# Kernel optimization log

Measured on AMD Instinct MI355X. Metric: run time of the kernel, lower is better.

The kernel has to match this reference:

```python
import jax, jax.numpy as jnp
import numpy as np

N = 16384
K = 16

def _w(k, shape):
    return jax.random.normal(k, shape, jnp.float32) * 0.05

def setup_inputs() -> dict:
    key = jax.random.key(0)
    ks = jax.random.split(key, 20)
    return {
        "img_feat": jax.random.normal(ks[0], (1, 32, N), jnp.float32),
        "cloud": jax.random.uniform(ks[1], (1, N, 3), jnp.float32),
        "conv1_w": _w(ks[2], (64, 32)),   "conv1_b": _w(ks[3], (64,)),
        "conv2_w": _w(ks[4], (128, 64)),  "conv2_b": _w(ks[5], (128,)),
        "psconv1_w": _w(ks[6], (256, 128)), "psconv1_b": _w(ks[7], (256,)),
        "psconv2_w": _w(ks[8], (128, 256)), "psconv2_b": _w(ks[9], (128,)),
        "pconv1_w": _w(ks[10], (64, 3)),  "pconv1_b": _w(ks[11], (64,)),
        "pconv2_w": _w(ks[12], (128, 64)),"pconv2_b": _w(ks[13], (128,)),
        "final_w": _w(ks[14], (32, 416)), "final_b": _w(ks[15], (32,)),
        "topk": K,
    }

def reference(img_feat, cloud, conv1_w, conv1_b, conv2_w, conv2_b,
              psconv1_w, psconv1_b, psconv2_w, psconv2_b,
              pconv1_w, pconv1_b, pconv2_w, pconv2_b,
              final_w, final_b, topk):
    lrelu = lambda x: jax.nn.leaky_relu(x, 0.01)
    pts = cloud[0]            # [N,3]  (module assumes bs=1)
    imf = img_feat[0].T       # [N,32]
    # point MLP: pconv1 -> lrelu -> pconv2 (Conv1d kernel=1 == per-point linear)
    cf = lrelu(pts @ pconv1_w.T + pconv1_b) @ pconv2_w.T + pconv2_b  # [N,128]
    # KNN: k smallest euclidean distances (self included)
    sq = jnp.sum(pts * pts, axis=-1)                 # [N]
    d2 = sq[:, None] + sq[None, :] - 2.0 * (pts @ pts.T)  # [N,N]
    _, idx = jax.lax.top_k(-d2, topk)                # [N,K]
    nb_pts = pts[idx]                                # [N,K,3]
    dist = jnp.sqrt(jnp.maximum(jnp.sum((pts[:, None, :] - nb_pts) ** 2, -1), 1e-12))
    wgt = jax.nn.softmax(-dist, axis=1)              # [N,K]
    nb_img = imf[idx]                                # [N,K,32]
    nb_cf = cf[idx]                                  # [N,K,128]
    sf = lrelu(nb_img @ conv1_w.T + conv1_b) @ conv2_w.T + conv2_b         # [N,K,128]
    sfp = lrelu(nb_cf @ psconv1_w.T + psconv1_b) @ psconv2_w.T + psconv2_b # [N,K,128]
    sf = jnp.max(sf * wgt[:, :, None], axis=1)       # weighted max-pool -> [N,128]
    sfp = jnp.max(sfp * wgt[:, :, None], axis=1)     # [N,128]
    final = jnp.concatenate([sfp, imf, sf, cf], axis=1)  # [N,416]
    out = lrelu(final) @ final_w.T + final_b         # [N,32]
    return out.T[None]                               # [1,32,N]
```

## Files before the change

kernel.cpp:

```cpp
#include <hip/hip_runtime.h>
#include <math.h>

#define N 16384
#define KNN 16
#define G 14
#define NCELL (G * G * G)

typedef __attribute__((ext_vector_type(8))) short bf16x8;
typedef __attribute__((ext_vector_type(4))) float f32x4;
typedef unsigned short ushort_t;
typedef unsigned long long u64;

__device__ __forceinline__ float lrelu(float a) { return a > 0.f ? a : 0.01f * a; }

__device__ __forceinline__ ushort_t f2bf(float f) {
  unsigned u = __float_as_uint(f);
  u += 0x7FFF + ((u >> 16) & 1);
  return (ushort_t)(u >> 16);
}
__device__ __forceinline__ float bf2f(ushort_t h) {
  return __uint_as_float((unsigned)h << 16);
}
__device__ __forceinline__ float bflo(unsigned u) {
  return __uint_as_float(u << 16);
}
__device__ __forceinline__ float bfhi(unsigned u) {
  return __uint_as_float(u & 0xffff0000u);
}
__device__ __forceinline__ int lanerank(u64 mask) {
  return __builtin_amdgcn_mbcnt_hi((unsigned)(mask >> 32),
         __builtin_amdgcn_mbcnt_lo((unsigned)mask, 0));
}
__device__ __forceinline__ int cellof(float x) {
  int c = (int)(x * (float)G);
  return c < 0 ? 0 : (c > G - 1 ? G - 1 : c);
}
__device__ __forceinline__ int cellid(float x, float y, float z) {
  return (cellof(z) * G + cellof(y)) * G + cellof(x);
}

#define PPB 64
__global__ __launch_bounds__(256) void prepw_kernel(
    const float* __restrict__ img, const float* __restrict__ cloud,
    const float* __restrict__ p1w, const float* __restrict__ p1b,
    const float* __restrict__ p2w, const float* __restrict__ p2b,
    const float* __restrict__ ps1w, const float* __restrict__ ps2w,
    const float* __restrict__ c1w, const float* __restrict__ c2w,
    const float* __restrict__ fw,
    float4* __restrict__ pts4, ushort_t* __restrict__ cfh,
    ushort_t* __restrict__ imfh,
    ushort_t* __restrict__ w1h, ushort_t* __restrict__ w2h,
    ushort_t* __restrict__ c1h, ushort_t* __restrict__ c2h,
    ushort_t* __restrict__ fwh, int* __restrict__ count) {
  int t = threadIdx.x;
  if (blockIdx.x >= 256) {
    int e = (blockIdx.x - 256) * 256 + t;
    if (e < 32768) w1h[e] = f2bf(ps1w[e]);
    else if (e < 65536) w2h[e - 32768] = f2bf(ps2w[e - 32768]);
    else if (e < 67584) c1h[e - 65536] = f2bf(c1w[e - 65536]);
    else if (e < 75776) c2h[e - 67584] = f2bf(c2w[e - 67584]);
    else if (e < 89088) {
      int e2 = e - 75776;
      if (e2 < 13312) fwh[e2] = f2bf(fw[e2]);
    }
    return;
  }
  __shared__ alignas(16) float w2t[64 * 132];
  __shared__ alignas(16) float hs[PPB * 68];
  __shared__ alignas(16) float w1s[192];
  __shared__ alignas(16) float b1s[64];
  __shared__ alignas(16) float b2s[128];
  __shared__ alignas(16) ushort_t imt[PPB * 40];
  __shared__ float ptmp[PPB * 3];
  __shared__ float psx[PPB], psy[PPB], psz[PPB];
  int pb = blockIdx.x * PPB;

  for (int e = t; e < 128 * 64; e += 256) {
    int ch = e >> 6, k = e & 63;
    w2t[k * 132 + ch] = p2w[e];
  }
  if (t < 192) w1s[t] = p1w[t];
  if (t < 64) b1s[t] = p1b[t];
  if (t < 128) b2s[t] = p2b[t];
  if (t < PPB * 3) ptmp[t] = cloud[pb * 3 + t];
  __syncthreads();
  if (t < PPB) {
    float x = ptmp[t * 3], y = ptmp[t * 3 + 1], z = ptmp[t * 3 + 2];
    psx[t] = x; psy[t] = y; psz[t] = z;
    pts4[pb + t] = make_float4(x, y, z, x * x + y * y + z * z);
    atomicAdd(&count[cellid(x, y, z)], 1);
  }
  for (int e = t; e < 32 * PPB; e += 256) {
    int c = e >> 6, p = e & 63;
    imt[p * 40 + c] = f2bf(img[(size_t)c * N + pb + p]);
  }
  __syncthreads();
  {
    int p = t >> 2, c8 = (t & 3) << 3;
    *(uint4*)&imfh[(size_t)(pb + p) * 32 + c8] =
        *(const uint4*)&imt[p * 40 + c8];
  }
  for (int e = t; e < PPB * 64; e += 256) {
    int pt_ = e >> 6, ch = e & 63;
    float a = b1s[ch] + psx[pt_] * w1s[ch * 3] + psy[pt_] * w1s[ch * 3 + 1] +
              psz[pt_] * w1s[ch * 3 + 2];
    hs[pt_ * 68 + ch] = lrelu(a);
  }
  __syncthreads();
  for (int e = t; e < PPB * 32; e += 256) {
    int pt_ = e >> 5, c4 = (e & 31) << 2;
    float4 acc = *(const float4*)&b2s[c4];
    const float* hrow = &hs[pt_ * 68];
    #pragma unroll
    for (int k = 0; k < 64; k += 4) {
      float4 h4 = *(const float4*)&hrow[k];
      float4 w0 = *(const float4*)&w2t[(k + 0) * 132 + c4];
      float4 w1_ = *(const float4*)&w2t[(k + 1) * 132 + c4];
      float4 w2_ = *(const float4*)&w2t[(k + 2) * 132 + c4];
      float4 w3 = *(const float4*)&w2t[(k + 3) * 132 + c4];
      acc.x = fmaf(h4.x, w0.x, fmaf(h4.y, w1_.x, fmaf(h4.z, w2_.x, fmaf(h4.w, w3.x, acc.x))));
      acc.y = fmaf(h4.x, w0.y, fmaf(h4.y, w1_.y, fmaf(h4.z, w2_.y, fmaf(h4.w, w3.y, acc.y))));
      acc.z = fmaf(h4.x, w0.z, fmaf(h4.y, w1_.z, fmaf(h4.z, w2_.z, fmaf(h4.w, w3.z, acc.z))));
      acc.w = fmaf(h4.x, w0.w, fmaf(h4.y, w1_.w, fmaf(h4.z, w2_.w, fmaf(h4.w, w3.w, acc.w))));
    }
    unsigned lo = (unsigned)f2bf(acc.x) | ((unsigned)f2bf(acc.y) << 16);
    unsigned hi = (unsigned)f2bf(acc.z) | ((unsigned)f2bf(acc.w) << 16);
    *(uint2*)&cfh[(size_t)(pb + pt_) * 128 + c4] = make_uint2(lo, hi);
  }
}

__global__ __launch_bounds__(256) void scan_kernel(
    const int* __restrict__ count, int* __restrict__ cellStart,
    int* __restrict__ cellofs) {
  __shared__ int part[256];
  int t = threadIdx.x;
  int local[11];
  int s = 0;
  #pragma unroll
  for (int j = 0; j < 11; ++j) {
    int idx = t * 11 + j;
    local[j] = s;
    s += (idx < NCELL) ? count[idx] : 0;
  }
  part[t] = s;
  __syncthreads();
  for (int off = 1; off < 256; off <<= 1) {
    int v = (t >= off) ? part[t - off] : 0;
    __syncthreads();
    part[t] += v;
    __syncthreads();
  }
  int base = part[t] - s;
  #pragma unroll
  for (int j = 0; j < 11; ++j) {
    int idx = t * 11 + j;
    int v = base + local[j];
    if (idx < NCELL) { cellStart[idx] = v; cellofs[idx] = v; }
  }
  if (t == 255) cellStart[NCELL] = part[255];
}

__global__ __launch_bounds__(256) void scatter_kernel(
    const float4* __restrict__ pts4, int* __restrict__ cellofs,
    float4* __restrict__ spts) {
  int p = blockIdx.x * 256 + threadIdx.x;
  float4 v = pts4[p];
  int pos = atomicAdd(&cellofs[cellid(v.x, v.y, v.z)], 1);
  spts[pos] = make_float4(v.x, v.y, v.z, __int_as_float(p));
}

#define NB_LD 136
#define S1_LD 264
#define NI_LD 40
#define H1_LD 72
__global__ __launch_bounds__(256) void ymlp_kernel(
    const ushort_t* __restrict__ cfh, const ushort_t* __restrict__ imfh,
    const ushort_t* __restrict__ w1h, const float* __restrict__ b1,
    const ushort_t* __restrict__ w2h, const float* __restrict__ b2,
    const ushort_t* __restrict__ c1h, const float* __restrict__ c1b,
    const ushort_t* __restrict__ c2h, const float* __restrict__ c2b,
    ushort_t* __restrict__ ycf, ushort_t* __restrict__ yimg) {
  __shared__ alignas(16) ushort_t nb[64 * NB_LD];
  __shared__ alignas(16) ushort_t s1[64 * S1_LD];
  int t = threadIdx.x;
  int w = t >> 6, lane = t & 63;
  int col = lane & 15, quad = lane >> 4;

  if (blockIdx.x < 256) {
    int pbase = blockIdx.x * 64;
    for (int e = t; e < 1024; e += 256) {
      int row = e >> 4, c8 = (e & 15) << 3;
      *(uint4*)&nb[row * NB_LD + c8] =
          *(const uint4*)&cfh[(size_t)(pbase + row) * 128 + c8];
    }
    __syncthreads();
    f32x4 acc1[4][4];
    #pragma unroll
    for (int tt = 0; tt < 4; ++tt)
      #pragma unroll
      for (int p = 0; p < 4; ++p) acc1[tt][p] = (f32x4){0.f, 0.f, 0.f, 0.f};
    for (int k0 = 0; k0 < 128; k0 += 32) {
      bf16x8 a[4];
      #pragma unroll
      for (int p = 0; p < 4; ++p)
        a[p] = *(const bf16x8*)&nb[(p * 16 + col) * NB_LD + k0 + quad * 8];
      #pragma unroll
      for (int tt = 0; tt < 4; ++tt) {
        int n = w * 64 + tt * 16 + col;
        bf16x8 b = *(const bf16x8*)&w1h[n * 128 + k0 + quad * 8];
        #pragma unroll
        for (int p = 0; p < 4; ++p)
          acc1[tt][p] = __builtin_amdgcn_mfma_f32_16x16x32_bf16(a[p], b, acc1[tt][p], 0, 0, 0);
      }
    }
    #pragma unroll
    for (int tt = 0; tt < 4; ++tt) {
      int n = w * 64 + tt * 16 + col;
      float bb = b1[n];
      #pragma unroll
      for (int p = 0; p < 4; ++p)
        #pragma unroll
        for (int r = 0; r < 4; ++r)
          s1[(p * 16 + quad * 4 + r) * S1_LD + n] = f2bf(lrelu(acc1[tt][p][r] + bb));
    }
    __syncthreads();
    f32x4 acc2[2][4];
    #pragma unroll
    for (int tt = 0; tt < 2; ++tt)
      #pragma unroll
      for (int p = 0; p < 4; ++p) acc2[tt][p] = (f32x4){0.f, 0.f, 0.f, 0.f};
    for (int k0 = 0; k0 < 256; k0 += 32) {
      bf16x8 a[4];
      #pragma unroll
      for (int p = 0; p < 4; ++p)
        a[p] = *(const bf16x8*)&s1[(p * 16 + col) * S1_LD + k0 + quad * 8];
      #pragma unroll
      for (int tt = 0; tt < 2; ++tt) {
        int n = w * 32 + tt * 16 + col;
        bf16x8 b = *(const bf16x8*)&w2h[n * 256 + k0 + quad * 8];
        #pragma unroll
        for (int p = 0; p < 4; ++p)
          acc2[tt][p] = __builtin_amdgcn_mfma_f32_16x16x32_bf16(a[p], b, acc2[tt][p], 0, 0, 0);
      }
    }
    #pragma unroll
    for (int tt = 0; tt < 2; ++tt) {
      int n = w * 32 + tt * 16 + col;
      float bb = b2[n];
      #pragma unroll
      for (int p = 0; p < 4; ++p)
        #pragma unroll
        for (int r = 0; r < 4; ++r)
          nb[(p * 16 + quad * 4 + r) * NB_LD + n] = f2bf(acc2[tt][p][r] + bb);
    }
    __syncthreads();
    for (int e = t; e < 1024; e += 256) {
      int row = e >> 4, c8 = (e & 15) << 3;
      *(uint4*)&ycf[(size_t)(pbase + row) * 128 + c8] =
          *(const uint4*)&nb[row * NB_LD + c8];
    }
  } else {
    int pbase = (blockIdx.x - 256) * 64;
    ushort_t* nbi = nb;
    ushort_t* h1 = s1;
    {
      int row = t >> 2, c8 = (t & 3) << 3;
      *(uint4*)&nbi[row * NI_LD + c8] =
          *(const uint4*)&imfh[(size_t)(pbase + row) * 32 + c8];
    }
    __syncthreads();
    {
      f32x4 accA[4];
      #pragma unroll
      for (int p = 0; p < 4; ++p) accA[p] = (f32x4){0.f, 0.f, 0.f, 0.f};
      int n = w * 16 + col;
      bf16x8 b = *(const bf16x8*)&c1h[n * 32 + quad * 8];
      #pragma unroll
      for (int p = 0; p < 4; ++p) {
        bf16x8 a = *(const bf16x8*)&nbi[(p * 16 + col) * NI_LD + quad * 8];
        accA[p] = __builtin_amdgcn_mfma_f32_16x16x32_bf16(a, b, accA[p], 0, 0, 0);
      }
      __syncthreads();
      float bb = c1b[n];
      #pragma unroll
      for (int p = 0; p < 4; ++p)
        #pragma unroll
        for (int r = 0; r < 4; ++r)
          h1[(p * 16 + quad * 4 + r) * H1_LD + n] = f2bf(lrelu(accA[p][r] + bb));
    }
    __syncthreads();
    f32x4 acc2[2][4];
    #pragma unroll
    for (int tt = 0; tt < 2; ++tt)
      #pragma unroll
      for (int p = 0; p < 4; ++p) acc2[tt][p] = (f32x4){0.f, 0.f, 0.f, 0.f};
    for (int k0 = 0; k0 < 64; k0 += 32) {
      bf16x8 a[4];
      #pragma unroll
      for (int p = 0; p < 4; ++p)
        a[p] = *(const bf16x8*)&h1[(p * 16 + col) * H1_LD + k0 + quad * 8];
      #pragma unroll
      for (int tt = 0; tt < 2; ++tt) {
        int n = w * 32 + tt * 16 + col;
        bf16x8 b = *(const bf16x8*)&c2h[n * 64 + k0 + quad * 8];
        #pragma unroll
        for (int p = 0; p < 4; ++p)
          acc2[tt][p] = __builtin_amdgcn_mfma_f32_16x16x32_bf16(a[p], b, acc2[tt][p], 0, 0, 0);
      }
    }
    #pragma unroll
    for (int tt = 0; tt < 2; ++tt) {
      int n = w * 32 + tt * 16 + col;
      float bb = c2b[n];
      #pragma unroll
      for (int p = 0; p < 4; ++p)
        #pragma unroll
        for (int r = 0; r < 4; ++r)
          nb[(p * 16 + quad * 4 + r) * NB_LD + n] = f2bf(acc2[tt][p][r] + bb);
    }
    __syncthreads();
    for (int e = t; e < 1024; e += 256) {
      int row = e >> 4, c8 = (e & 15) << 3;
      *(uint4*)&yimg[(size_t)(pbase + row) * 128 + c8] =
          *(const uint4*)&nb[row * NB_LD + c8];
    }
  }
}

__device__ __forceinline__ float tadj(float tau, float qw) {
  float a = tau - qw;
  return a + fabsf(a) * 2e-7f + 1e-35f;
}

template <int NS>
__device__ __forceinline__ u64 selimpl(u64* buf, int cnt, int lane,
                                       float& tau) {
  u64 v[NS];
  unsigned k[NS];
  #pragma unroll
  for (int s = 0; s < NS; ++s) {
    int idx = s * 64 + lane;
    v[s] = (idx < cnt) ? buf[idx] : ~0ULL;
    k[s] = (unsigned)(v[s] >> 32);
  }
  unsigned m = 0u;
  #pragma unroll
  for (int b = 31; b >= 0; --b) {
    unsigned probe = m | (1u << b);
    int c = 0;
    #pragma unroll
    for (int s = 0; s < NS; ++s) c += __popcll(__ballot(k[s] < probe));
    if (c < KNN) m = probe;
  }
  int c_lt = 0, ne = 0;
  bool e[NS];
  #pragma unroll
  for (int s = 0; s < NS; ++s) {
    c_lt += __popcll(__ballot(k[s] < m));
    e[s] = (k[s] == m);
    ne += __popcll(__ballot(e[s]));
  }
  int need_eq = KNN - c_lt;
  unsigned m2 = 0xFFFFFFFFu;
  if (ne != need_eq) {
    m2 = 0u;
    #pragma unroll
    for (int b = 13; b >= 0; --b) {
      unsigned probe = m2 | (1u << b);
      int c = 0;
      #pragma unroll
      for (int s = 0; s < NS; ++s)
        c += __popcll(__ballot(e[s] && ((unsigned)v[s] < probe)));
      if (c < need_eq) m2 = probe;
    }
  }
  int base = 0;
  #pragma unroll
  for (int s = 0; s < NS; ++s) {
    bool sel = (k[s] < m) || (e[s] && ((unsigned)v[s] <= m2));
    u64 msk = __ballot(sel);
    if (sel) buf[base + lanerank(msk)] = v[s];
    base += __popcll(msk);
  }
  tau = __uint_as_float(m);
  if (!(tau == tau)) tau = INFINITY;
  return buf[lane & 15];
}

__device__ __forceinline__ u64 select16(u64* buf, int& cnt, int lane,
                                        float& tau) {
  u64 r = (cnt <= 64) ? selimpl<1>(buf, cnt, lane, tau)
                      : selimpl<2>(buf, cnt, lane, tau);
  cnt = KNN;
  return r;
}

__global__ __launch_bounds__(256) void knng_kernel(
    const float4* __restrict__ spts, const int* __restrict__ cellStart,
    const ushort_t* __restrict__ ycf, const ushort_t* __restrict__ yimg,
    const ushort_t* __restrict__ cfh, const ushort_t* __restrict__ imfh,
    ushort_t* __restrict__ featb) {
  __shared__ u64 sbuf[4][128];
  __shared__ alignas(16) float feat[4][416];
  int t = threadIdx.x;
  int wv = t >> 6, lane = t & 63;
  int sblk = (blockIdx.x & 7) * 512 + (blockIdx.x >> 3);
  int sid = sblk * 4 + wv;
  u64* buf = sbuf[wv];

  float4 q = spts[sid];
  int pid = __float_as_int(q.w);
  float qw = fmaf(q.z, q.z, fmaf(q.y, q.y, q.x * q.x));
  float q2x = -2.f * q.x, q2y = -2.f * q.y, q2z = -2.f * q.z;
  int cx = cellof(q.x), cy = cellof(q.y), cz = cellof(q.z);

  float tau;
  {
    const float r0 = 0.0758f;
    float rr = r0;
    #pragma unroll
    for (int it = 0; it < 2; ++it) {
      float fx = (fminf(q.x + rr, 1.f) - fmaxf(q.x - rr, 0.f)) * (0.5f / rr);
      float fy = (fminf(q.y + rr, 1.f) - fmaxf(q.y - rr, 0.f)) * (0.5f / rr);
      float fz = (fminf(q.z + rr, 1.f) - fmaxf(q.z - rr, 0.f)) * (0.5f / rr);
      rr = r0 * __powf(fx * fy * fz, -0.333333f);
    }
    rr *= 1.05f;
    tau = rr * rr;
  }
  u64 vres;

  for (int r = 1;; ++r) {
    int lx = max(cx - r, 0), hx = min(cx + r, G - 1);
    int ly = max(cy - r, 0), hy = min(cy + r, G - 1);
    int lz = max(cz - r, 0), hz = min(cz + r, G - 1);
    int ny = hy - ly + 1, nz = hz - lz + 1, nruns = ny * nz;
    int cnt = 0;
    float ta = tadj(tau, qw);

    for (int rb = 0; rb < nruns; rb += 64) {
      int ln = rb + lane;
      int rs = 0, rc = 0;
      if (ln < nruns) {
        int z = lz + ln / ny, y = ly + ln % ny;
        int row = (z * G + y) * G;
        rs = cellStart[row + lx];
        rc = cellStart[row + hx + 1] - rs;
      }
      int nr = nruns - rb; nr = nr > 64 ? 64 : nr;
      int off = rc;
      #pragma unroll
      for (int d = 1; d < 64; d <<= 1) {
        int v = __shfl_up(off, d);
        if (lane >= d) off += v;
      }
      int T = __shfl(off, 63);
      off -= rc;

      for (int cb = 0; cb < T; cb += 64) {
        int rk = cb + lane;
        int j = 0;
        if (nr <= 16) {
          #pragma unroll
          for (int step = 8; step; step >>= 1) {
            int nj = j + step;
            if (__shfl(off, nj) <= rk) j = nj;
          }
        } else if (nr <= 32) {
          #pragma unroll
          for (int step = 16; step; step >>= 1) {
            int nj = j + step;
            if (__shfl(off, nj) <= rk) j = nj;
          }
        } else {
          #pragma unroll
          for (int step = 32; step; step >>= 1) {
            int nj = j + step;
            if (__shfl(off, nj) <= rk) j = nj;
          }
        }
        int src = __shfl(rs, j) + rk - __shfl(off, j);
        bool valid = rk < T;
        if (!valid) src = 0;
        float4 c = spts[src];
        float cw = fmaf(c.z, c.z, fmaf(c.y, c.y, c.x * c.x));
        float d2 = fmaf(q2x, c.x, fmaf(q2y, c.y, fmaf(q2z, c.z, cw)));
        bool pass = valid && (d2 <= ta);
        u64 mask = __ballot(pass);
        if (mask) {
          if (pass) {
            int oid = __float_as_int(c.w);
            u64 key = ((u64)__float_as_uint(fmaxf(d2 + qw, 0.f)) << 32) | (unsigned)oid;
            buf[cnt + lanerank(mask)] = key;
          }
          cnt += __popcll(mask);
          if (cnt > 64) {
            select16(buf, cnt, lane, tau);
            ta = tadj(tau, qw);
          }
        }
      }
    }
    u64 v = select16(buf, cnt, lane, tau);
    float cl = INFINITY;
    if (lx > 0)     cl = fminf(cl, q.x - (float)lx / (float)G);
    if (hx < G - 1) cl = fminf(cl, (float)(hx + 1) / (float)G - q.x);
    if (ly > 0)     cl = fminf(cl, q.y - (float)ly / (float)G);
    if (hy < G - 1) cl = fminf(cl, (float)(hy + 1) / (float)G - q.y);
    if (lz > 0)     cl = fminf(cl, q.z - (float)lz / (float)G);
    if (hz < G - 1) cl = fminf(cl, (float)(hz + 1) / (float)G - q.z);
    bool full = (lx == 0 && hx == G - 1 && ly == 0 && hy == G - 1 &&
                 lz == 0 && hz == G - 1);
    if (full || tau * 1.00002f <= cl * cl) { vres = v; break; }
  }

  int myid = (lane < KNN) ? (int)(unsigned)(vres & 0xffffffffULL) : 0;
  float mywg = 0.f;
  {
    float dd = __uint_as_float((unsigned)(vres >> 32));
    float dist = sqrtf(fmaxf(dd, 1e-12f));
    float md = (lane < KNN) ? dist : INFINITY;
    #pragma unroll
    for (int off = 1; off < KNN; off <<= 1) md = fminf(md, __shfl_xor(md, off));
    float e = __expf(md - dist);
    float se = (lane < KNN) ? e : 0.f;
    #pragma unroll
    for (int off = 1; off < KNN; off <<= 1) se += __shfl_xor(se, off);
    mywg = e / se;
  }

  int ksub = lane >> 4, c8 = lane & 15;
  float vimf = (lane < 32) ? bf2f(imfh[(size_t)pid * 32 + lane]) : 0.f;
  unsigned vcf = *(const unsigned*)&cfh[(size_t)pid * 128 + lane * 2];

  float a0[8], a1[8];
  #pragma unroll
  for (int j = 0; j < 8; ++j) { a0[j] = -INFINITY; a1[j] = -INFINITY; }
  #pragma unroll
  for (int kk = 0; kk < 4; ++kk) {
    int k = kk * 4 + ksub;
    int id = __shfl(myid, k);
    float wg = __shfl(mywg, k);
    uint4 v = *(const uint4*)&ycf[(size_t)id * 128 + c8 * 8];
    uint4 u = *(const uint4*)&yimg[(size_t)id * 128 + c8 * 8];
    unsigned vv[4] = {v.x, v.y, v.z, v.w};
    unsigned uu[4] = {u.x, u.y, u.z, u.w};
    #pragma unroll
    for (int h = 0; h < 4; ++h) {
      a0[h * 2]     = fmaxf(a0[h * 2],     bflo(vv[h]) * wg);
      a0[h * 2 + 1] = fmaxf(a0[h * 2 + 1], bfhi(vv[h]) * wg);
      a1[h * 2]     = fmaxf(a1[h * 2],     bflo(uu[h]) * wg);
      a1[h * 2 + 1] = fmaxf(a1[h * 2 + 1], bfhi(uu[h]) * wg);
    }
  }
  #pragma unroll
  for (int j = 0; j < 8; ++j) {
    a0[j] = fmaxf(a0[j], __shfl_xor(a0[j], 16));
    a0[j] = fmaxf(a0[j], __shfl_xor(a0[j], 32));
    a1[j] = fmaxf(a1[j], __shfl_xor(a1[j], 16));
    a1[j] = fmaxf(a1[j], __shfl_xor(a1[j], 32));
  }
  if (lane < 16) {
    #pragma unroll
    for (int j = 0; j < 8; ++j) {
      feat[wv][c8 * 8 + j] = lrelu(a0[j]);
      feat[wv][160 + c8 * 8 + j] = lrelu(a1[j]);
    }
  }
  if (lane < 32) feat[wv][128 + lane] = lrelu(vimf);
  feat[wv][288 + lane * 2] = lrelu(bflo(vcf));
  feat[wv][288 + lane * 2 + 1] = lrelu(bfhi(vcf));

  unsigned* frow = (unsigned*)(featb + (size_t)pid * 416);
  #pragma unroll
  for (int it = 0; it < 4; ++it) {
    int pi = it * 64 + lane;
    if (pi < 208) {
      float lo = feat[wv][pi * 2], hi = feat[wv][pi * 2 + 1];
      frow[pi] = (unsigned)f2bf(lo) | ((unsigned)f2bf(hi) << 16);
    }
  }
}

__global__ __launch_bounds__(256) void fing_kernel(
    const ushort_t* __restrict__ featb, const ushort_t* __restrict__ fwh,
    const float* __restrict__ fb, float* __restrict__ out) {
  int t = threadIdx.x;
  int wv = t >> 6, lane = t & 63;
  int col = lane & 15, quad = lane >> 4;
  int pbase = blockIdx.x * 64 + wv * 16;
  f32x4 acc[2];
  acc[0] = (f32x4){0.f, 0.f, 0.f, 0.f};
  acc[1] = (f32x4){0.f, 0.f, 0.f, 0.f};
  for (int k0 = 0; k0 < 416; k0 += 32) {
    bf16x8 b = *(const bf16x8*)&featb[(size_t)(pbase + col) * 416 + k0 + quad * 8];
    #pragma unroll
    for (int tt = 0; tt < 2; ++tt) {
      bf16x8 a = *(const bf16x8*)&fwh[(tt * 16 + col) * 416 + k0 + quad * 8];
      acc[tt] = __builtin_amdgcn_mfma_f32_16x16x32_bf16(a, b, acc[tt], 0, 0, 0);
    }
  }
  #pragma unroll
  for (int tt = 0; tt < 2; ++tt) {
    #pragma unroll
    for (int r = 0; r < 4; ++r) {
      int ch = tt * 16 + quad * 4 + r;
      out[(size_t)ch * N + pbase + col] = acc[tt][r] + fb[ch];
    }
  }
}

extern "C" void kernel_launch(void* const* d_in, const int* in_sizes, int n_in,
                              void* d_out, int out_size, void* d_ws, size_t ws_size,
                              hipStream_t stream) {
  const float* img   = (const float*)d_in[0];
  const float* cloud = (const float*)d_in[1];
  const float* c1w   = (const float*)d_in[2];
  const float* c1b   = (const float*)d_in[3];
  const float* c2w   = (const float*)d_in[4];
  const float* c2b   = (const float*)d_in[5];
  const float* ps1w  = (const float*)d_in[6];
  const float* ps1b  = (const float*)d_in[7];
  const float* ps2w  = (const float*)d_in[8];
  const float* ps2b  = (const float*)d_in[9];
  const float* p1w   = (const float*)d_in[10];
  const float* p1b   = (const float*)d_in[11];
  const float* p2w   = (const float*)d_in[12];
  const float* p2b   = (const float*)d_in[13];
  const float* fw    = (const float*)d_in[14];
  const float* fb    = (const float*)d_in[15];
  float* out = (float*)d_out;

  char* ws = (char*)d_ws;
  float4*   pts4  = (float4*)(ws + 0);
  ushort_t* cfh   = (ushort_t*)(ws + 262144);
  ushort_t* imfh  = (ushort_t*)(ws + 4456448);
  ushort_t* w1h   = (ushort_t*)(ws + 5505024);
  ushort_t* w2h   = (ushort_t*)(ws + 5570560);
  ushort_t* c1h   = (ushort_t*)(ws + 5636096);
  ushort_t* c2h   = (ushort_t*)(ws + 5640192);
  ushort_t* ycf   = (ushort_t*)(ws + 5656576);
  ushort_t* yimg  = (ushort_t*)(ws + 9850880);
  float4*   spts  = (float4*)(ws + 14045184);
  int*      cellStart = (int*)(ws + 14307328);
  int*      cellofs   = (int*)(ws + 14323712);
  int*      count     = (int*)(ws + 14339840);
  ushort_t* fwh       = (ushort_t*)(ws + 14356224);
  ushort_t* featb     = (ushort_t*)(ws + 14388992);

  hipMemsetAsync(count, 0, NCELL * sizeof(int), stream);
  prepw_kernel<<<604, 256, 0, stream>>>(img, cloud, p1w, p1b, p2w, p2b,
                                        ps1w, ps2w, c1w, c2w, fw,
                                        pts4, cfh, imfh, w1h, w2h, c1h, c2h,
                                        fwh, count);
  scan_kernel<<<1, 256, 0, stream>>>(count, cellStart, cellofs);
  scatter_kernel<<<64, 256, 0, stream>>>(pts4, cellofs, spts);
  ymlp_kernel<<<512, 256, 0, stream>>>(cfh, imfh, w1h, ps1b, w2h, ps2b,
                                       c1h, c1b, c2h, c2b, ycf, yimg);
  knng_kernel<<<N / 4, 256, 0, stream>>>(spts, cellStart,
                                         ycf, yimg, cfh, imfh, featb);
  fing_kernel<<<N / 64, 256, 0, stream>>>(featb, fwh, fb, out);
}
```

Baseline: 170.5 us.

## Clip KNN cell runs to sphere radius and simplify neighbour feature gather

```diff
diff --git a/kernel.cpp b/kernel.cpp
--- a/kernel.cpp
+++ b/kernel.cpp
@@ -395,13 +395,16 @@
   return r;
 }
 
+__device__ __forceinline__ float truethr(float tau, float qw) {
+  return tau + (tau + qw) * 3e-7f + 1e-30f;
+}
+
 __global__ __launch_bounds__(256) void knng_kernel(
     const float4* __restrict__ spts, const int* __restrict__ cellStart,
     const ushort_t* __restrict__ ycf, const ushort_t* __restrict__ yimg,
     const ushort_t* __restrict__ cfh, const ushort_t* __restrict__ imfh,
     ushort_t* __restrict__ featb) {
   __shared__ u64 sbuf[4][128];
-  __shared__ alignas(16) float feat[4][416];
   int t = threadIdx.x;
   int wv = t >> 6, lane = t & 63;
   int sblk = (blockIdx.x & 7) * 512 + (blockIdx.x >> 3);
@@ -437,15 +440,26 @@
     int ny = hy - ly + 1, nz = hz - lz + 1, nruns = ny * nz;
     int cnt = 0;
     float ta = tadj(tau, qw);
+    float tt = truethr(tau, qw);
 
     for (int rb = 0; rb < nruns; rb += 64) {
       int ln = rb + lane;
       int rs = 0, rc = 0;
       if (ln < nruns) {
         int z = lz + ln / ny, y = ly + ln % ny;
-        int row = (z * G + y) * G;
-        rs = cellStart[row + lx];
-        rc = cellStart[row + hx + 1] - rs;
+        float loY = (float)y * (1.f / G), hiY = loY + (1.f / G);
+        float loZ = (float)z * (1.f / G), hiZ = loZ + (1.f / G);
+        float dy = fmaxf(fmaxf(loY - q.y, q.y - hiY) - 1e-6f, 0.f);
+        float dz = fmaxf(fmaxf(loZ - q.z, q.z - hiZ) - 1e-6f, 0.f);
+        float rem = tt - dy * dy - dz * dz;
+        if (rem >= 0.f) {
+          float rad = fminf(sqrtf(rem) + 1e-6f, 2.f);
+          int xlo = max(lx, cellof(q.x - rad));
+          int xhi = min(hx, cellof(q.x + rad));
+          int row = (z * G + y) * G;
+          rs = cellStart[row + xlo];
+          rc = cellStart[row + xhi + 1] - rs;
+        }
       }
       int nr = nruns - rb; nr = nr > 64 ? 64 : nr;
       int off = rc;
@@ -497,6 +511,7 @@
           if (cnt > 64) {
             select16(buf, cnt, lane, tau);
             ta = tadj(tau, qw);
+            tt = truethr(tau, qw);
           }
         }
       }
@@ -529,57 +544,30 @@
     mywg = e / se;
   }
 
-  int ksub = lane >> 4, c8 = lane & 15;
-  float vimf = (lane < 32) ? bf2f(imfh[(size_t)pid * 32 + lane]) : 0.f;
-  unsigned vcf = *(const unsigned*)&cfh[(size_t)pid * 128 + lane * 2];
-
-  float a0[8], a1[8];
-  #pragma unroll
-  for (int j = 0; j < 8; ++j) { a0[j] = -INFINITY; a1[j] = -INFINITY; }
-  #pragma unroll
-  for (int kk = 0; kk < 4; ++kk) {
-    int k = kk * 4 + ksub;
+  float A0 = -INFINITY, A1 = -INFINITY, B0 = -INFINITY, B1 = -INFINITY;
+  size_t coff = (size_t)(lane * 2);
+  #pragma unroll
+  for (int k = 0; k < KNN; ++k) {
     int id = __shfl(myid, k);
     float wg = __shfl(mywg, k);
-    uint4 v = *(const uint4*)&ycf[(size_t)id * 128 + c8 * 8];
-    uint4 u = *(const uint4*)&yimg[(size_t)id * 128 + c8 * 8];
-    unsigned vv[4] = {v.x, v.y, v.z, v.w};
-    unsigned uu[4] = {u.x, u.y, u.z, u.w};
-    #pragma unroll
-    for (int h = 0; h < 4; ++h) {
-      a0[h * 2]     = fmaxf(a0[h * 2],     bflo(vv[h]) * wg);
-      a0[h * 2 + 1] = fmaxf(a0[h * 2 + 1], bfhi(vv[h]) * wg);
-      a1[h * 2]     = fmaxf(a1[h * 2],     bflo(uu[h]) * wg);
-      a1[h * 2 + 1] = fmaxf(a1[h * 2 + 1], bfhi(uu[h]) * wg);
-    }
-  }
-  #pragma unroll
-  for (int j = 0; j < 8; ++j) {
-    a0[j] = fmaxf(a0[j], __shfl_xor(a0[j], 16));
-    a0[j] = fmaxf(a0[j], __shfl_xor(a0[j], 32));
-    a1[j] = fmaxf(a1[j], __shfl_xor(a1[j], 16));
-    a1[j] = fmaxf(a1[j], __shfl_xor(a1[j], 32));
-  }
+    unsigned v = *(const unsigned*)&ycf[(size_t)id * 128 + coff];
+    unsigned u = *(const unsigned*)&yimg[(size_t)id * 128 + coff];
+    A0 = fmaxf(A0, bflo(v) * wg);
+    A1 = fmaxf(A1, bfhi(v) * wg);
+    B0 = fmaxf(B0, bflo(u) * wg);
+    B1 = fmaxf(B1, bfhi(u) * wg);
+  }
+  unsigned* frow = (unsigned*)(featb + (size_t)pid * 416);
+  frow[lane] = (unsigned)f2bf(lrelu(A0)) | ((unsigned)f2bf(lrelu(A1)) << 16);
+  frow[80 + lane] = (unsigned)f2bf(lrelu(B0)) | ((unsigned)f2bf(lrelu(B1)) << 16);
   if (lane < 16) {
-    #pragma unroll
-    for (int j = 0; j < 8; ++j) {
-      feat[wv][c8 * 8 + j] = lrelu(a0[j]);
-      feat[wv][160 + c8 * 8 + j] = lrelu(a1[j]);
-    }
-  }
-  if (lane < 32) feat[wv][128 + lane] = lrelu(vimf);
-  feat[wv][288 + lane * 2] = lrelu(bflo(vcf));
-  feat[wv][288 + lane * 2 + 1] = lrelu(bfhi(vcf));
-
-  unsigned* frow = (unsigned*)(featb + (size_t)pid * 416);
-  #pragma unroll
-  for (int it = 0; it < 4; ++it) {
-    int pi = it * 64 + lane;
-    if (pi < 208) {
-      float lo = feat[wv][pi * 2], hi = feat[wv][pi * 2 + 1];
-      frow[pi] = (unsigned)f2bf(lo) | ((unsigned)f2bf(hi) << 16);
-    }
-  }
+    unsigned vi = *(const unsigned*)&imfh[(size_t)pid * 32 + lane * 2];
+    frow[64 + lane] =
+        (unsigned)f2bf(lrelu(bflo(vi))) | ((unsigned)f2bf(lrelu(bfhi(vi))) << 16);
+  }
+  unsigned vcf = *(const unsigned*)&cfh[(size_t)pid * 128 + coff];
+  frow[144 + lane] =
+      (unsigned)f2bf(lrelu(bflo(vcf))) | ((unsigned)f2bf(lrelu(bfhi(vcf))) << 16);
 }
 
 __global__ __launch_bounds__(256) void fing_kernel(
```

New measurement: 166.3 us. 2.5% less time.
